# Optimization experiments

Measured on AMD Instinct MI355X. Metric: run time of the kernel, lower is better.

## Reference

```python
import jax, jax.numpy as jnp
import numpy as np

NB_OBJ = 3
DIM_BODY = 10
DIM_OBJ = 15
DIM_LEMB = 100
PHI_IN = DIM_LEMB + DIM_BODY + 2 * (NB_OBJ + DIM_OBJ)  # 146
HID = 256
PHI_OUT = 256
ACT_DIM = 4
BATCH = 65536
LOG_SIG_MIN, LOG_SIG_MAX = -20.0, 2.0
# permutations of 3 objects taken 2: (0,1),(0,2),(1,0),(1,2),(2,0),(2,1)
IDX_I = np.array([0, 0, 1, 1, 2, 2])
IDX_J = np.array([1, 2, 0, 2, 0, 1])


def _xavier(key, fan_in, fan_out):
    lim = float(np.sqrt(6.0 / (fan_in + fan_out)))
    return jax.random.uniform(key, (fan_in, fan_out), jnp.float32, -lim, lim)


def setup_inputs() -> dict:
    key = jax.random.key(0)
    ks = jax.random.split(key, 8)
    return {
        "obs": jax.random.normal(ks[0], (BATCH, DIM_BODY + NB_OBJ * DIM_OBJ), jnp.float32),
        "l_emb": jax.random.normal(ks[1], (BATCH, DIM_LEMB), jnp.float32),
        "phi_w1": _xavier(ks[2], PHI_IN, HID), "phi_b1": jnp.zeros((HID,), jnp.float32),
        "phi_w2": _xavier(ks[3], HID, PHI_OUT), "phi_b2": jnp.zeros((PHI_OUT,), jnp.float32),
        "rho_w1": _xavier(ks[4], PHI_OUT, HID), "rho_b1": jnp.zeros((HID,), jnp.float32),
        "mean_w": _xavier(ks[5], HID, ACT_DIM), "mean_b": jnp.zeros((ACT_DIM,), jnp.float32),
        "lstd_w": _xavier(ks[6], HID, ACT_DIM), "lstd_b": jnp.zeros((ACT_DIM,), jnp.float32),
    }


def reference(obs, l_emb, phi_w1, phi_b1, phi_w2, phi_b2,
              rho_w1, rho_b1, mean_w, mean_b, lstd_w, lstd_b):
    B = obs.shape[0]
    obs_body = obs[:, :DIM_BODY]                                   # [B, 10]
    obj_feats = obs[:, DIM_BODY:].reshape(B, NB_OBJ, DIM_OBJ)      # [B, 3, 15]
    one_hot = jnp.broadcast_to(jnp.eye(NB_OBJ, dtype=obs.dtype)[None], (B, NB_OBJ, NB_OBJ))
    objs = jnp.concatenate([one_hot, obj_feats], axis=-1)          # [B, 3, 18]
    base = jnp.concatenate([l_emb, obs_body], axis=-1)             # [B, 110]
    # pairwise concat over the 6 ordered pairs -> [6, B, 146]
    xi = objs[:, IDX_I].transpose(1, 0, 2)                         # [6, B, 18]
    xj = objs[:, IDX_J].transpose(1, 0, 2)
    base6 = jnp.broadcast_to(base[None], (6, B, base.shape[-1]))
    inp = jnp.concatenate([base6, xi, xj], axis=-1)                # [6, B, 146]
    # phi MLP
    h = jax.nn.relu(jnp.einsum('pbi,ih->pbh', inp, phi_w1) + phi_b1)
    h = jax.nn.relu(jnp.einsum('pbh,ho->pbo', h, phi_w2) + phi_b2)
    agg = h.sum(axis=0)                                            # [B, 256]
    # rho MLP
    r = jax.nn.relu(agg @ rho_w1 + rho_b1)
    mean = r @ mean_w + mean_b
    log_std = jnp.clip(r @ lstd_w + lstd_b, LOG_SIG_MIN, LOG_SIG_MAX)
    return mean, log_std
```

## Files before the change

kernel.cpp:

```cpp
#include <hip/hip_runtime.h>

#define BATCH 65536
#define TB 32

typedef _Float16 half8 __attribute__((ext_vector_type(8)));
typedef _Float16 half4v __attribute__((ext_vector_type(4)));
typedef _Float16 half2v __attribute__((ext_vector_type(2)));
typedef float fx4 __attribute__((ext_vector_type(4)));

#define PW1B_OFF 0
#define PW1F_OFF 32768
#define PW2_OFF  40960
#define PWR_OFF  106496
#define PWH_OFF  172032
#define WS_TOTAL 176128

__global__ __launch_bounds__(256) void prep_weights(
    const float* __restrict__ w1, const float* __restrict__ w2,
    const float* __restrict__ wr, const float* __restrict__ wm,
    const float* __restrict__ wl, _Float16* __restrict__ ws)
{
  int idx = blockIdx.x * 256 + threadIdx.x;
  if (idx < 32768) {
    int kk = idx & 31, n = (idx >> 5) & 255, kt = idx >> 13;
    int k = kt * 32 + kk;
    ws[idx] = (k < 110) ? (_Float16)w1[k * 256 + n] : (_Float16)0.f;
  } else if (idx < 40960) {
    int t = idx - 32768;
    int kk = t & 31, n = t >> 5;
    _Float16 v = (_Float16)0.f;
    if (kk < 15)                  v = (_Float16)w1[(113 + kk) * 256 + n];
    else if (kk >= 16 && kk < 31) v = (_Float16)w1[(131 + (kk - 16)) * 256 + n];
    ws[idx] = v;
  } else if (idx < 106496) {
    int t = idx - 40960;
    int kk = t & 31, n = (t >> 5) & 255, kt = t >> 13;
    ws[idx] = (_Float16)w2[(kt * 32 + kk) * 256 + n];
  } else if (idx < 172032) {
    int t = idx - 106496;
    int kk = t & 31, n = (t >> 5) & 255, kt = t >> 13;
    ws[idx] = (_Float16)wr[(kt * 32 + kk) * 256 + n];
  } else if (idx < WS_TOTAL) {
    int t = idx - 172032;
    int kk = t & 31, n = (t >> 5) & 15, kt = t >> 9;
    int k = kt * 32 + kk;
    _Float16 v = (_Float16)0.f;
    if (n < 4) v = (_Float16)wm[k * 4 + n];
    else if (n < 8) v = (_Float16)wl[k * 4 + (n - 4)];
    ws[PWH_OFF + t] = v;
  }
}

__global__ __launch_bounds__(512, 4) void actor_fused(
    const float* __restrict__ obs, const float* __restrict__ lemb,
    const float* __restrict__ w1, const _Float16* __restrict__ ws,
    const float* __restrict__ b1, const float* __restrict__ b2,
    const float* __restrict__ br, const float* __restrict__ bm,
    const float* __restrict__ bl, float* __restrict__ out)
{
  __shared__ __align__(16) _Float16 H1[6 * 16 * 256];
  __shared__ __align__(16) _Float16 Bb[32 * 256];
  __shared__ __align__(16) _Float16 Os[3 * 32 * 16];
  __shared__ __align__(16) float    Bsf[6 * 256];

  const _Float16* __restrict__ pw1b = ws + PW1B_OFF;
  const _Float16* __restrict__ pw1f = ws + PW1F_OFF;
  const _Float16* __restrict__ pw2  = ws + PW2_OFF;
  const _Float16* __restrict__ pwr  = ws + PWR_OFF;
  const _Float16* __restrict__ pwh  = ws + PWH_OFF;

  const int tid  = threadIdx.x;
  const int wave = tid >> 6;
  const int lane = tid & 63;
  const int q    = lane >> 4;
  const int l16  = lane & 15;
  const int colbase = wave * 32;
  const int rowbase = blockIdx.x * TB;

  const int c0_0 = colbase + q * 4;
  const int c0_1 = colbase + 16 + q * 4;

  for (int idx = tid; idx < 2048; idx += 512) {
    int r = idx >> 6, c2 = idx & 63, c = c2 * 2;
    float v0 = 0.f, v1 = 0.f;
    if (c2 < 50) {
      float2 v = ((const float2*)(lemb + (rowbase + r) * 100))[c2];
      v0 = v.x; v1 = v.y;
    } else if (c < 110) {
      v0 = obs[(rowbase + r) * 55 + (c - 100)];
      v1 = (c + 1 < 110) ? obs[(rowbase + r) * 55 + (c - 99)] : 0.f;
    }
    half2v hv = {(_Float16)v0, (_Float16)v1};
    *(half2v*)&Bb[((c >> 3) * 32 + r) * 8 + (c & 7)] = hv;
  }
  for (int idx = tid; idx < 1536; idx += 512) {
    int o = idx >> 9, rem = idx & 511, r = rem >> 4, k = rem & 15;
    float v = (k < 15) ? obs[(rowbase + r) * 55 + 10 + o * 15 + k] : 0.f;
    Os[o * 512 + ((k >> 3) * 32 + r) * 8 + (k & 7)] = (_Float16)v;
  }
  for (int idx = tid; idx < 1536; idx += 512) {
    int p = idx >> 8, c = idx & 255;
    int oi = p >> 1, oj = (1161 >> (2 * p)) & 3;
    Bsf[idx] = b1[c] + w1[(110 + oi) * 256 + c] + w1[(128 + oj) * 256 + c];
  }
  __syncthreads();

  const fx4 zero4 = {0.f, 0.f, 0.f, 0.f};

  fx4 u[4];
  u[0] = zero4; u[1] = zero4; u[2] = zero4; u[3] = zero4;
  #pragma unroll
  for (int kt = 0; kt < 4; ++kt) {
    half8 a0 = *(const half8*)&Bb[((kt * 4 + q) * 32 + l16) * 8];
    half8 a1 = *(const half8*)&Bb[((kt * 4 + q) * 32 + 16 + l16) * 8];
    #pragma unroll
    for (int nt = 0; nt < 2; ++nt) {
      half8 b = *(const half8*)&pw1b[(kt * 256 + colbase + nt * 16 + l16) * 32 + q * 8];
      u[nt]     = __builtin_amdgcn_mfma_f32_16x16x32_f16(b, a0, u[nt], 0, 0, 0);
      u[2 + nt] = __builtin_amdgcn_mfma_f32_16x16x32_f16(b, a1, u[2 + nt], 0, 0, 0);
    }
  }

  auto g1_group = [&](int g) {
    half8 b1f0 = *(const half8*)&pw1f[(colbase + l16) * 32 + q * 8];
    half8 b1f1 = *(const half8*)&pw1f[(colbase + 16 + l16) * 32 + q * 8];
    #pragma unroll
    for (int pp = 0; pp < 3; ++pp) {
      const int p = g * 3 + pp;
      const int oi = p >> 1, oj = (1161 >> (2 * p)) & 3;
      const int o = (q < 2) ? oi : oj;
      #pragma unroll
      for (int rt = 0; rt < 2; ++rt) {
        half8 af = *(const half8*)&Os[o * 512 + ((q & 1) * 32 + rt * 16 + l16) * 8];
        #pragma unroll
        for (int nt = 0; nt < 2; ++nt) {
          fx4 t = __builtin_amdgcn_mfma_f32_16x16x32_f16(nt ? b1f1 : b1f0, af,
                                                         u[rt * 2 + nt], 0, 0, 0);
          const int c0 = nt ? c0_1 : c0_0;
          fx4 bs = *(const fx4*)&Bsf[p * 256 + c0];
          float h0 = fmaxf(t[0] + bs[0], 0.f);
          float h1v = fmaxf(t[1] + bs[1], 0.f);
          float h2v = fmaxf(t[2] + bs[2], 0.f);
          float h3v = fmaxf(t[3] + bs[3], 0.f);
          half4v hv = {(_Float16)h0, (_Float16)h1v, (_Float16)h2v, (_Float16)h3v};
          *(half4v*)&H1[(pp * 2 + rt) * 4096 + ((c0 >> 3) * 16 + l16) * 8 + (c0 & 7)] = hv;
        }
      }
    }
  };

  fx4 agg[4];
  agg[0] = zero4; agg[1] = zero4; agg[2] = zero4; agg[3] = zero4;
  fx4 b2v[2];
  b2v[0] = *(const fx4*)&b2[c0_0];
  b2v[1] = *(const fx4*)&b2[c0_1];

  auto g2_group = [&]() {
    fx4 acc[12];
    #pragma unroll
    for (int i = 0; i < 12; ++i) acc[i] = b2v[i & 1];
    #pragma unroll 2
    for (int kt = 0; kt < 8; ++kt) {
      half8 bb0 = *(const half8*)&pw2[(kt * 256 + colbase + l16) * 32 + q * 8];
      half8 bb1 = *(const half8*)&pw2[(kt * 256 + colbase + 16 + l16) * 32 + q * 8];
      #pragma unroll
      for (int t6 = 0; t6 < 6; ++t6) {
        half8 a = *(const half8*)&H1[t6 * 4096 + ((kt * 4 + q) * 16 + l16) * 8];
        acc[t6 * 2]     = __builtin_amdgcn_mfma_f32_16x16x32_f16(bb0, a, acc[t6 * 2], 0, 0, 0);
        acc[t6 * 2 + 1] = __builtin_amdgcn_mfma_f32_16x16x32_f16(bb1, a, acc[t6 * 2 + 1], 0, 0, 0);
      }
    }
    #pragma unroll
    for (int t6 = 0; t6 < 6; ++t6)
      #pragma unroll
      for (int nt = 0; nt < 2; ++nt)
        #pragma unroll
        for (int rr = 0; rr < 4; ++rr) {
          float h = acc[t6 * 2 + nt][rr];
          if (h > 0.f) agg[(t6 & 1) * 2 + nt][rr] += h;
        }
  };

  g1_group(0);
  __syncthreads();
  g2_group();
  __syncthreads();
  g1_group(1);
  __syncthreads();
  g2_group();

  #pragma unroll
  for (int rt = 0; rt < 2; ++rt)
    #pragma unroll
    for (int nt = 0; nt < 2; ++nt) {
      const int c0 = nt ? c0_1 : c0_0;
      fx4 t = agg[rt * 2 + nt];
      half4v hv = {(_Float16)t[0], (_Float16)t[1], (_Float16)t[2], (_Float16)t[3]};
      *(half4v*)&Bb[((c0 >> 3) * 32 + rt * 16 + l16) * 8 + (c0 & 7)] = hv;
    }
  __syncthreads();

  fx4 acc3[4];
  {
    fx4 brv0 = *(const fx4*)&br[c0_0];
    fx4 brv1 = *(const fx4*)&br[c0_1];
    acc3[0] = brv0; acc3[1] = brv1; acc3[2] = brv0; acc3[3] = brv1;
  }
  #pragma unroll 2
  for (int kt = 0; kt < 8; ++kt) {
    half8 a0 = *(const half8*)&Bb[((kt * 4 + q) * 32 + l16) * 8];
    half8 a1 = *(const half8*)&Bb[((kt * 4 + q) * 32 + 16 + l16) * 8];
    #pragma unroll
    for (int nt = 0; nt < 2; ++nt) {
      half8 b = *(const half8*)&pwr[(kt * 256 + colbase + nt * 16 + l16) * 32 + q * 8];
      acc3[nt]     = __builtin_amdgcn_mfma_f32_16x16x32_f16(b, a0, acc3[nt], 0, 0, 0);
      acc3[2 + nt] = __builtin_amdgcn_mfma_f32_16x16x32_f16(b, a1, acc3[2 + nt], 0, 0, 0);
    }
  }
  #pragma unroll
  for (int rt = 0; rt < 2; ++rt)
    #pragma unroll
    for (int nt = 0; nt < 2; ++nt) {
      const int c0 = nt ? c0_1 : c0_0;
      fx4 t = acc3[rt * 2 + nt];
      half4v hv = {(_Float16)fmaxf(t[0], 0.f), (_Float16)fmaxf(t[1], 0.f),
                   (_Float16)fmaxf(t[2], 0.f), (_Float16)fmaxf(t[3], 0.f)};
      *(half4v*)&H1[rt * 4096 + ((c0 >> 3) * 16 + l16) * 8 + (c0 & 7)] = hv;
    }
  __syncthreads();

  if (wave < 2) {
    fx4 a4 = zero4;
    #pragma unroll 2
    for (int kt = 0; kt < 8; ++kt) {
      half8 rfrag = *(const half8*)&H1[wave * 4096 + ((kt * 4 + q) * 16 + l16) * 8];
      half8 wfrag = *(const half8*)&pwh[(kt * 16 + l16) * 32 + q * 8];
      a4 = __builtin_amdgcn_mfma_f32_16x16x32_f16(wfrag, rfrag, a4, 0, 0, 0);
    }
    const int row = rowbase + wave * 16 + l16;
    if (q == 0) {
      fx4 bm4 = *(const fx4*)bm;
      fx4 o = {a4[0] + bm4[0], a4[1] + bm4[1], a4[2] + bm4[2], a4[3] + bm4[3]};
      *(fx4*)&out[row * 4] = o;
    } else if (q == 1) {
      fx4 bl4 = *(const fx4*)bl;
      fx4 o;
      #pragma unroll
      for (int rr = 0; rr < 4; ++rr) {
        float v = a4[rr] + bl4[rr];
        o[rr] = v < -20.f ? -20.f : (v > 2.f ? 2.f : v);
      }
      *(fx4*)&out[BATCH * 4 + row * 4] = o;
    }
  }
}

extern "C" void kernel_launch(void* const* d_in, const int* in_sizes, int n_in,
                              void* d_out, int out_size, void* d_ws, size_t ws_size,
                              hipStream_t stream) {
  const float* obs  = (const float*)d_in[0];
  const float* lemb = (const float*)d_in[1];
  const float* w1   = (const float*)d_in[2];
  const float* b1   = (const float*)d_in[3];
  const float* w2   = (const float*)d_in[4];
  const float* b2   = (const float*)d_in[5];
  const float* wr   = (const float*)d_in[6];
  const float* br   = (const float*)d_in[7];
  const float* wm   = (const float*)d_in[8];
  const float* bm   = (const float*)d_in[9];
  const float* wl   = (const float*)d_in[10];
  const float* bl   = (const float*)d_in[11];
  float* out = (float*)d_out;
  _Float16* ws = (_Float16*)d_ws;

  hipLaunchKernelGGL(prep_weights, dim3(WS_TOTAL / 256), dim3(256), 0, stream,
                     w1, w2, wr, wm, wl, ws);
  hipLaunchKernelGGL(actor_fused, dim3(BATCH / TB), dim3(512), 0, stream,
                     obs, lemb, w1, (const _Float16*)ws, b1, b2, br, bm, bl, out);
}
```

Measured before the change: 189.1 us.

## Vectorize input staging, fully unroll MFMA loops, and adjust waves-per-EU hint

Staging of the l_emb/obs rows into shared memory now uses float4 loads and half4 stores, so fewer threads do wider accesses. The phi layer-2, rho and head MFMA loops are fully unrolled, with all six H1 A-fragments loaded before the MFMAs to expose more LDS parallelism. The conditional ReLU accumulate becomes a branch-free fmaxf. The launch-bounds occupancy hint is replaced by amdgpu_waves_per_eu(4,4). Together these aim to cut load-instruction count and scheduling stalls, at the cost of higher register pressure.

```diff
diff --git a/kernel.cpp b/kernel.cpp
--- a/kernel.cpp
+++ b/kernel.cpp
@@ -51,7 +51,8 @@
   }
 }
 
-__global__ __launch_bounds__(512, 4) void actor_fused(
+__global__ __launch_bounds__(512) __attribute__((amdgpu_waves_per_eu(4, 4)))
+void actor_fused(
     const float* __restrict__ obs, const float* __restrict__ lemb,
     const float* __restrict__ w1, const _Float16* __restrict__ ws,
     const float* __restrict__ b1, const float* __restrict__ b2,
@@ -80,23 +81,43 @@
   const int c0_0 = colbase + q * 4;
   const int c0_1 = colbase + 16 + q * 4;
 
-  for (int idx = tid; idx < 2048; idx += 512) {
-    int r = idx >> 6, c2 = idx & 63, c = c2 * 2;
-    float v0 = 0.f, v1 = 0.f;
-    if (c2 < 50) {
-      float2 v = ((const float2*)(lemb + (rowbase + r) * 100))[c2];
-      v0 = v.x; v1 = v.y;
-    } else if (c < 110) {
-      v0 = obs[(rowbase + r) * 55 + (c - 100)];
-      v1 = (c + 1 < 110) ? obs[(rowbase + r) * 55 + (c - 99)] : 0.f;
-    }
-    half2v hv = {(_Float16)v0, (_Float16)v1};
-    *(half2v*)&Bb[((c >> 3) * 32 + r) * 8 + (c & 7)] = hv;
-  }
-  for (int idx = tid; idx < 1536; idx += 512) {
-    int o = idx >> 9, rem = idx & 511, r = rem >> 4, k = rem & 15;
-    float v = (k < 15) ? obs[(rowbase + r) * 55 + 10 + o * 15 + k] : 0.f;
-    Os[o * 512 + ((k >> 3) * 32 + r) * 8 + (k & 7)] = (_Float16)v;
+  for (int idx = tid; idx < 1024; idx += 512) {
+    int oct = idx >> 6;
+    int r   = (idx >> 1) & 31;
+    int hf  = idx & 1;
+    int c   = oct * 8 + hf * 4;
+    float v0, v1, v2, v3;
+    if (c + 3 < 100) {
+      float4 f = *(const float4*)(lemb + (rowbase + r) * 100 + c);
+      v0 = f.x; v1 = f.y; v2 = f.z; v3 = f.w;
+    } else {
+      const float* orow = obs + (rowbase + r) * 55;
+      const float* lrow = lemb + (rowbase + r) * 100;
+      float t[4];
+      #pragma unroll
+      for (int j = 0; j < 4; ++j) {
+        int cc = c + j;
+        t[j] = cc < 100 ? lrow[cc] : (cc < 110 ? orow[cc - 100] : 0.f);
+      }
+      v0 = t[0]; v1 = t[1]; v2 = t[2]; v3 = t[3];
+    }
+    half4v hv = {(_Float16)v0, (_Float16)v1, (_Float16)v2, (_Float16)v3};
+    *(half4v*)&Bb[(oct * 32 + r) * 8 + hf * 4] = hv;
+  }
+  for (int idx = tid; idx < 384; idx += 512) {
+    int o   = idx >> 7;
+    int k4i = (idx >> 5) & 3;
+    int r   = idx & 31;
+    int k0  = k4i * 4;
+    const float* frow = obs + (rowbase + r) * 55 + 10 + o * 15;
+    float t[4];
+    #pragma unroll
+    for (int j = 0; j < 4; ++j) {
+      int k = k0 + j;
+      t[j] = (k < 15) ? frow[k] : 0.f;
+    }
+    half4v hv = {(_Float16)t[0], (_Float16)t[1], (_Float16)t[2], (_Float16)t[3]};
+    *(half4v*)&Os[o * 512 + ((k0 >> 3) * 32 + r) * 8 + (k0 & 7)] = hv;
   }
   for (int idx = tid; idx < 1536; idx += 512) {
     int p = idx >> 8, c = idx & 255;
@@ -138,11 +159,10 @@
                                                          u[rt * 2 + nt], 0, 0, 0);
           const int c0 = nt ? c0_1 : c0_0;
           fx4 bs = *(const fx4*)&Bsf[p * 256 + c0];
-          float h0 = fmaxf(t[0] + bs[0], 0.f);
-          float h1v = fmaxf(t[1] + bs[1], 0.f);
-          float h2v = fmaxf(t[2] + bs[2], 0.f);
-          float h3v = fmaxf(t[3] + bs[3], 0.f);
-          half4v hv = {(_Float16)h0, (_Float16)h1v, (_Float16)h2v, (_Float16)h3v};
+          half4v hv = {(_Float16)fmaxf(t[0] + bs[0], 0.f),
+                       (_Float16)fmaxf(t[1] + bs[1], 0.f),
+                       (_Float16)fmaxf(t[2] + bs[2], 0.f),
+                       (_Float16)fmaxf(t[3] + bs[3], 0.f)};
           *(half4v*)&H1[(pp * 2 + rt) * 4096 + ((c0 >> 3) * 16 + l16) * 8 + (c0 & 7)] = hv;
         }
       }
@@ -151,23 +171,27 @@
 
   fx4 agg[4];
   agg[0] = zero4; agg[1] = zero4; agg[2] = zero4; agg[3] = zero4;
-  fx4 b2v[2];
-  b2v[0] = *(const fx4*)&b2[c0_0];
-  b2v[1] = *(const fx4*)&b2[c0_1];
 
   auto g2_group = [&]() {
+    const _Float16* wp0 = &pw2[(colbase + l16) * 32 + q * 8];
+    const _Float16* wp1 = wp0 + 16 * 32;
+    fx4 bv0 = *(const fx4*)&b2[c0_0];
+    fx4 bv1 = *(const fx4*)&b2[c0_1];
     fx4 acc[12];
     #pragma unroll
-    for (int i = 0; i < 12; ++i) acc[i] = b2v[i & 1];
-    #pragma unroll 2
+    for (int i = 0; i < 12; ++i) acc[i] = (i & 1) ? bv1 : bv0;
+    #pragma unroll
     for (int kt = 0; kt < 8; ++kt) {
-      half8 bb0 = *(const half8*)&pw2[(kt * 256 + colbase + l16) * 32 + q * 8];
-      half8 bb1 = *(const half8*)&pw2[(kt * 256 + colbase + 16 + l16) * 32 + q * 8];
+      half8 a[6];
+      #pragma unroll
+      for (int t6 = 0; t6 < 6; ++t6)
+        a[t6] = *(const half8*)&H1[t6 * 4096 + ((kt * 4 + q) * 16 + l16) * 8];
+      half8 bb0 = *(const half8*)(wp0 + kt * 8192);
+      half8 bb1 = *(const half8*)(wp1 + kt * 8192);
       #pragma unroll
       for (int t6 = 0; t6 < 6; ++t6) {
-        half8 a = *(const half8*)&H1[t6 * 4096 + ((kt * 4 + q) * 16 + l16) * 8];
-        acc[t6 * 2]     = __builtin_amdgcn_mfma_f32_16x16x32_f16(bb0, a, acc[t6 * 2], 0, 0, 0);
-        acc[t6 * 2 + 1] = __builtin_amdgcn_mfma_f32_16x16x32_f16(bb1, a, acc[t6 * 2 + 1], 0, 0, 0);
+        acc[t6 * 2]     = __builtin_amdgcn_mfma_f32_16x16x32_f16(bb0, a[t6], acc[t6 * 2], 0, 0, 0);
+        acc[t6 * 2 + 1] = __builtin_amdgcn_mfma_f32_16x16x32_f16(bb1, a[t6], acc[t6 * 2 + 1], 0, 0, 0);
       }
     }
     #pragma unroll
@@ -175,10 +199,8 @@
       #pragma unroll
       for (int nt = 0; nt < 2; ++nt)
         #pragma unroll
-        for (int rr = 0; rr < 4; ++rr) {
-          float h = acc[t6 * 2 + nt][rr];
-          if (h > 0.f) agg[(t6 & 1) * 2 + nt][rr] += h;
-        }
+        for (int rr = 0; rr < 4; ++rr)
+          agg[(t6 & 1) * 2 + nt][rr] += fmaxf(acc[t6 * 2 + nt][rr], 0.f);
   };
 
   g1_group(0);
@@ -206,16 +228,16 @@
     fx4 brv1 = *(const fx4*)&br[c0_1];
     acc3[0] = brv0; acc3[1] = brv1; acc3[2] = brv0; acc3[3] = brv1;
   }
-  #pragma unroll 2
+  #pragma unroll
   for (int kt = 0; kt < 8; ++kt) {
     half8 a0 = *(const half8*)&Bb[((kt * 4 + q) * 32 + l16) * 8];
     half8 a1 = *(const half8*)&Bb[((kt * 4 + q) * 32 + 16 + l16) * 8];
-    #pragma unroll
-    for (int nt = 0; nt < 2; ++nt) {
-      half8 b = *(const half8*)&pwr[(kt * 256 + colbase + nt * 16 + l16) * 32 + q * 8];
-      acc3[nt]     = __builtin_amdgcn_mfma_f32_16x16x32_f16(b, a0, acc3[nt], 0, 0, 0);
-      acc3[2 + nt] = __builtin_amdgcn_mfma_f32_16x16x32_f16(b, a1, acc3[2 + nt], 0, 0, 0);
-    }
+    half8 b0 = *(const half8*)&pwr[(kt * 256 + colbase + l16) * 32 + q * 8];
+    half8 b1h = *(const half8*)&pwr[(kt * 256 + colbase + 16 + l16) * 32 + q * 8];
+    acc3[0] = __builtin_amdgcn_mfma_f32_16x16x32_f16(b0,  a0, acc3[0], 0, 0, 0);
+    acc3[1] = __builtin_amdgcn_mfma_f32_16x16x32_f16(b1h, a0, acc3[1], 0, 0, 0);
+    acc3[2] = __builtin_amdgcn_mfma_f32_16x16x32_f16(b0,  a1, acc3[2], 0, 0, 0);
+    acc3[3] = __builtin_amdgcn_mfma_f32_16x16x32_f16(b1h, a1, acc3[3], 0, 0, 0);
   }
   #pragma unroll
   for (int rt = 0; rt < 2; ++rt)
@@ -231,7 +253,7 @@
 
   if (wave < 2) {
     fx4 a4 = zero4;
-    #pragma unroll 2
+    #pragma unroll
     for (int kt = 0; kt < 8; ++kt) {
       half8 rfrag = *(const half8*)&H1[wave * 4096 + ((kt * 4 + q) * 16 + l16) * 8];
       half8 wfrag = *(const half8*)&pwh[(kt * 16 + l16) * 32 + q * 8];
```

Measured after the change: 204.9 us. 1.08x slower.
